# Kernel optimization log

Measured on AMD Instinct MI355X. Metric: run time of the kernel, lower is better.

Reference implementation:

```python
import jax, jax.numpy as jnp
import numpy as np

B, S, D, H = 2, 2048, 1024, 16
DK = D // H


def setup_inputs() -> dict:
    key = jax.random.key(0)
    ks = jax.random.split(key, 12)
    scale = 1.0 / np.sqrt(D)
    inp = {
        "Q": jax.random.normal(ks[0], (B, S, D), jnp.float32),
        "K": jax.random.normal(ks[1], (B, S, D), jnp.float32),
        "V": jax.random.normal(ks[2], (B, S, D), jnp.float32),
        "mask": jnp.tril(jnp.ones((S, S), jnp.int32))[None, None],  # [1,1,S,S] causal
        "Wq": jax.random.normal(ks[3], (D, D), jnp.float32) * scale,
        "bq": jnp.zeros((D,), jnp.float32),
        "Wk": jax.random.normal(ks[4], (D, D), jnp.float32) * scale,
        "bk": jnp.zeros((D,), jnp.float32),
        "Wv": jax.random.normal(ks[5], (D, D), jnp.float32) * scale,
        "bv": jnp.zeros((D,), jnp.float32),
        "Wo": jax.random.normal(ks[6], (D, D), jnp.float32) * scale,
        "bo": jnp.zeros((D,), jnp.float32),
    }
    return inp


def _split_heads(x):
    # [B,S,D] -> [B,H,S,DK]
    b, s, _ = x.shape
    return x.reshape(b, s, H, DK).transpose(0, 2, 1, 3)


def reference(Q, K, V, mask, Wq, bq, Wk, bk, Wv, bv, Wo, bo):
    # Linear projections (torch Linear: x @ W.T + b)
    q = _split_heads(Q @ Wq.T + bq)
    k = _split_heads(K @ Wk.T + bk)
    v = _split_heads(V @ Wv.T + bv)
    scores = jnp.einsum("bhqd,bhkd->bhqk", q, k) / np.sqrt(DK).astype(np.float32)
    scores = jnp.where(mask == 0, jnp.float32(-1e9), scores)
    attn = jax.nn.softmax(scores, axis=-1)
    out = jnp.einsum("bhqk,bhkd->bhqd", attn, v)
    out = out.transpose(0, 2, 1, 3).reshape(Q.shape[0], Q.shape[1], D)  # combine heads
    out = out @ Wo.T + bo
    return out, attn
```

## Files before the change

kernel.cpp:

```cpp
#include <hip/hip_runtime.h>
#include <hip/hip_bf16.h>
#include <math.h>

#define B_ 2
#define S_ 2048
#define D_ 1024
#define H_ 16
#define DK_ 64

typedef __bf16 bf16_t;
typedef __bf16 bf16x8 __attribute__((ext_vector_type(8)));
typedef __bf16 bf16x4 __attribute__((ext_vector_type(4)));
typedef float f32x4 __attribute__((ext_vector_type(4)));

__device__ __forceinline__ void gload_lds16(const void* g, void* l) {
    __builtin_amdgcn_global_load_lds(
        (const __attribute__((address_space(1))) unsigned int*)g,
        (__attribute__((address_space(3))) unsigned int*)l, 16, 0, 0);
}

__global__ __launch_bounds__(256) void cvt_kernel(
    const float* __restrict__ Q, const float* __restrict__ K, const float* __restrict__ V,
    const float* __restrict__ Wq, const float* __restrict__ Wk,
    const float* __restrict__ Wv, const float* __restrict__ Wo,
    bf16_t* __restrict__ dst)
{
    int gid = blockIdx.x * 256 + threadIdx.x;
    for (int i = gid; i < 2097152; i += 2048 * 256) {
        const float* src;
        size_t soff;
        if (i < 1572864) {
            int s = i >> 19;
            src = (s == 0) ? Q : (s == 1) ? K : V;
            soff = (size_t)(i - (s << 19)) * 8;
        } else {
            int j = i - 1572864;
            int s = j >> 17;
            src = (s == 0) ? Wq : (s == 1) ? Wk : (s == 2) ? Wv : Wo;
            soff = (size_t)(j & 131071) * 8;
        }
        float4 a = *(const float4*)(src + soff);
        float4 b = *(const float4*)(src + soff + 4);
        bf16x8 o;
        o[0] = (bf16_t)a.x; o[1] = (bf16_t)a.y; o[2] = (bf16_t)a.z; o[3] = (bf16_t)a.w;
        o[4] = (bf16_t)b.x; o[5] = (bf16_t)b.y; o[6] = (bf16_t)b.z; o[7] = (bf16_t)b.w;
        *(bf16x8*)(dst + (size_t)i * 8) = o;
    }
}

__global__ __launch_bounds__(256) void qkv_gemm_kernel(
    const bf16_t* __restrict__ xq, const bf16_t* __restrict__ xk, const bf16_t* __restrict__ xv,
    const bf16_t* __restrict__ wqb, const bf16_t* __restrict__ wkb, const bf16_t* __restrict__ wvb,
    const float* __restrict__ bq, const float* __restrict__ bk, const float* __restrict__ bv,
    bf16_t* __restrict__ qws, bf16_t* __restrict__ kws, bf16_t* __restrict__ vws)
{
    __shared__ __align__(16) bf16_t As[2][128 * 32];
    __shared__ __align__(16) bf16_t Bs[2][128 * 32];

    const int z = blockIdx.z;
    const bf16_t* A  = (z == 0) ? xq : (z == 1) ? xk : xv;
    const bf16_t* Wb = (z == 0) ? wqb : (z == 1) ? wkb : wvb;
    const float* bias = (z == 0) ? bq : (z == 1) ? bk : bv;
    bf16_t* out       = (z == 0) ? qws : (z == 1) ? kws : vws;

    const int tid = threadIdx.x;
    const int lane = tid & 63, w = tid >> 6;
    const int lr = lane & 15, lg = lane >> 4;
    const int wr = w >> 1, wc = w & 1;
    const int m0 = blockIdx.y * 128, n0 = blockIdx.x * 128;
    const int sr = lane >> 2;
    const int sc = (lane & 3) * 8;

    f32x4 acc[4][4] = {};

    auto stage = [&](int p, int kt) {
        #pragma unroll
        for (int i = 0; i < 2; ++i) {
            int row = w * 32 + i * 16;
            gload_lds16(&A[(size_t)(m0 + row + sr) * 1024 + kt + sc], &As[p][row * 32]);
            gload_lds16(&Wb[(size_t)(n0 + row + sr) * 1024 + kt + sc], &Bs[p][row * 32]);
        }
    };

    stage(0, 0);
    __syncthreads();
    int p = 0;
    for (int kt = 0; kt < 1024; kt += 32) {
        if (kt + 32 < 1024) stage(p ^ 1, kt + 32);
        bf16x8 af[4], bfr[4];
        #pragma unroll
        for (int mi = 0; mi < 4; ++mi)
            af[mi] = *(const bf16x8*)&As[p][(wr * 64 + mi * 16 + lr) * 32 + lg * 8];
        #pragma unroll
        for (int ni = 0; ni < 4; ++ni)
            bfr[ni] = *(const bf16x8*)&Bs[p][(wc * 64 + ni * 16 + lr) * 32 + lg * 8];
        #pragma unroll
        for (int mi = 0; mi < 4; ++mi)
            #pragma unroll
            for (int ni = 0; ni < 4; ++ni)
                acc[mi][ni] = __builtin_amdgcn_mfma_f32_16x16x32_bf16(af[mi], bfr[ni], acc[mi][ni], 0, 0, 0);
        __syncthreads();
        p ^= 1;
    }

    #pragma unroll
    for (int mi = 0; mi < 4; ++mi) {
        int mrow = m0 + wr * 64 + mi * 16 + lg * 4;
        #pragma unroll
        for (int ni = 0; ni < 4; ++ni) {
            int n = n0 + wc * 64 + ni * 16 + lr;
            float bvl = bias[n];
            int h = n >> 6, dk = n & 63;
            #pragma unroll
            for (int r = 0; r < 4; ++r) {
                int m = mrow + r;
                int b = m >> 11, s = m & 2047;
                float val = acc[mi][ni][r] + bvl;
                if (z < 2) {
                    out[(((size_t)(b * H_ + h)) * S_ + s) * DK_ + dk] = (bf16_t)val;
                } else {
                    out[(((size_t)(b * H_ + h)) * DK_ + dk) * S_ + s] = (bf16_t)val;
                }
            }
        }
    }
}

__global__ __launch_bounds__(256, 2) void attn_kernel(
    const bf16_t* __restrict__ qws, const bf16_t* __restrict__ kws, const bf16_t* __restrict__ vws,
    float* __restrict__ attn_out, bf16_t* __restrict__ ctx)
{
    __shared__ __align__(16) bf16_t Ks[2][64][72];
    __shared__ __align__(16) bf16_t Vs[2][64][72];
    __shared__ __align__(16) bf16_t Ps[4][16][72];
    __shared__ __align__(16) float  Ps32[4][16][68];

    const int tid = threadIdx.x;
    const int lane = tid & 63, w = tid >> 6;
    const int lr = lane & 15, lg = lane >> 4;

    const int fid = blockIdx.x;
    const int xcd = fid & 7;
    const int slot = fid >> 3;
    const int bh = xcd * 4 + (slot >> 4);
    const int pr = slot & 15;
    const int b = bh >> 4, h = bh & 15;

    const bf16_t* qh = qws + (size_t)bh * S_ * DK_;
    const bf16_t* kh = kws + (size_t)bh * S_ * DK_;
    const bf16_t* vh = vws + (size_t)bh * DK_ * S_;
    float* ab = attn_out + (size_t)bh * S_ * S_;

    const float SCALE2 = 0.18033688011112042f;

    const int srow = tid >> 3;
    const int scol = (tid & 7) * 8;

    const int prow = lane >> 4;
    const int pcol = (lane & 15) * 4;

    #pragma unroll
    for (int half = 0; half < 2; ++half) {
        const int qt = half ? pr : 31 - pr;
        const int q0 = qt * 64;
        const int nt = qt + 1;
        const int qrow = q0 + w * 16 + lr;

        bf16x8 qf0 = *(const bf16x8*)&qh[(size_t)qrow * DK_ + lg * 8];
        bf16x8 qf1 = *(const bf16x8*)&qh[(size_t)qrow * DK_ + 32 + lg * 8];

        {
            uint4 c0 = *(const uint4*)&kh[(size_t)srow * DK_ + scol];
            uint4 c1 = *(const uint4*)&kh[(size_t)(srow + 32) * DK_ + scol];
            *(uint4*)&Ks[0][srow][scol] = c0;
            *(uint4*)&Ks[0][srow + 32][scol] = c1;
        }
        __syncthreads();
        int p = 0;
        float l = 0.0f;
        for (int t = 0; t < nt; ++t) {
            const bool pre = (t + 1 < nt);
            uint4 k0n, k1n;
            if (pre) {
                k0n = *(const uint4*)&kh[(size_t)((t + 1) * 64 + srow) * DK_ + scol];
                k1n = *(const uint4*)&kh[(size_t)((t + 1) * 64 + srow + 32) * DK_ + scol];
            }
            f32x4 sf[4] = {};
            #pragma unroll
            for (int fj = 0; fj < 4; ++fj) {
                bf16x8 a0 = *(const bf16x8*)&Ks[p][fj * 16 + lr][lg * 8];
                bf16x8 a1 = *(const bf16x8*)&Ks[p][fj * 16 + lr][32 + lg * 8];
                sf[fj] = __builtin_amdgcn_mfma_f32_16x16x32_bf16(a0, qf0, sf[fj], 0, 0, 0);
                sf[fj] = __builtin_amdgcn_mfma_f32_16x16x32_bf16(a1, qf1, sf[fj], 0, 0, 0);
            }
            if (t == qt) {
                #pragma unroll
                for (int fj = 0; fj < 4; ++fj)
                    #pragma unroll
                    for (int r = 0; r < 4; ++r) {
                        float s2 = sf[fj][r] * SCALE2;
                        if (t * 64 + fj * 16 + lg * 4 + r > qrow) s2 = -1e30f;
                        l += exp2f(s2);
                    }
            } else {
                #pragma unroll
                for (int fj = 0; fj < 4; ++fj)
                    #pragma unroll
                    for (int r = 0; r < 4; ++r)
                        l += exp2f(sf[fj][r] * SCALE2);
            }
            if (pre) {
                *(uint4*)&Ks[p ^ 1][srow][scol] = k0n;
                *(uint4*)&Ks[p ^ 1][srow + 32][scol] = k1n;
            }
            __syncthreads();
            p ^= 1;
        }
        l += __shfl_xor(l, 16, 64);
        l += __shfl_xor(l, 32, 64);
        const float csub = log2f(l);

        {
            uint4 c0 = *(const uint4*)&kh[(size_t)srow * DK_ + scol];
            uint4 c1 = *(const uint4*)&kh[(size_t)(srow + 32) * DK_ + scol];
            uint4 d0 = *(const uint4*)&vh[(size_t)srow * S_ + scol];
            uint4 d1 = *(const uint4*)&vh[(size_t)(srow + 32) * S_ + scol];
            *(uint4*)&Ks[0][srow][scol] = c0;
            *(uint4*)&Ks[0][srow + 32][scol] = c1;
            *(uint4*)&Vs[0][srow][scol] = d0;
            *(uint4*)&Vs[0][srow + 32][scol] = d1;
        }
        __syncthreads();
        p = 0;
        f32x4 oacc[4] = {};
        for (int t = 0; t < nt; ++t) {
            const bool pre = (t + 1 < nt);
            uint4 k0n, k1n, v0n, v1n;
            if (pre) {
                k0n = *(const uint4*)&kh[(size_t)((t + 1) * 64 + srow) * DK_ + scol];
                k1n = *(const uint4*)&kh[(size_t)((t + 1) * 64 + srow + 32) * DK_ + scol];
                v0n = *(const uint4*)&vh[(size_t)srow * S_ + (t + 1) * 64 + scol];
                v1n = *(const uint4*)&vh[(size_t)(srow + 32) * S_ + (t + 1) * 64 + scol];
            }
            f32x4 sf[4] = {};
            #pragma unroll
            for (int fj = 0; fj < 4; ++fj) {
                bf16x8 a0 = *(const bf16x8*)&Ks[p][fj * 16 + lr][lg * 8];
                bf16x8 a1 = *(const bf16x8*)&Ks[p][fj * 16 + lr][32 + lg * 8];
                sf[fj] = __builtin_amdgcn_mfma_f32_16x16x32_bf16(a0, qf0, sf[fj], 0, 0, 0);
                sf[fj] = __builtin_amdgcn_mfma_f32_16x16x32_bf16(a1, qf1, sf[fj], 0, 0, 0);
            }
            const bool diag = (t == qt);
            #pragma unroll
            for (int fj = 0; fj < 4; ++fj) {
                f32x4 pv;
                #pragma unroll
                for (int r = 0; r < 4; ++r) {
                    float s2 = sf[fj][r] * SCALE2;
                    if (diag && (t * 64 + fj * 16 + lg * 4 + r > qrow)) s2 = -1e30f;
                    pv[r] = exp2f(s2 - csub);
                }
                *(f32x4*)&Ps32[w][lr][fj * 16 + lg * 4] = pv;
                bf16x4 pb;
                #pragma unroll
                for (int r = 0; r < 4; ++r) pb[r] = (bf16_t)pv[r];
                *(bf16x4*)&Ps[w][lr][fj * 16 + lg * 4] = pb;
            }
            #pragma unroll
            for (int i = 0; i < 4; ++i) {
                int row = prow + i * 4;
                f32x4 pvt = *(const f32x4*)&Ps32[w][row][pcol];
                __builtin_nontemporal_store(pvt,
                    (f32x4*)&ab[(size_t)(q0 + w * 16 + row) * S_ + t * 64 + pcol]);
            }
            #pragma unroll
            for (int ks = 0; ks < 2; ++ks) {
                bf16x8 ap = *(const bf16x8*)&Ps[w][lr][ks * 32 + lg * 8];
                #pragma unroll
                for (int fd = 0; fd < 4; ++fd) {
                    bf16x8 bv = *(const bf16x8*)&Vs[p][fd * 16 + lr][ks * 32 + lg * 8];
                    oacc[fd] = __builtin_amdgcn_mfma_f32_16x16x32_bf16(ap, bv, oacc[fd], 0, 0, 0);
                }
            }
            if (pre) {
                *(uint4*)&Ks[p ^ 1][srow][scol] = k0n;
                *(uint4*)&Ks[p ^ 1][srow + 32][scol] = k1n;
                *(uint4*)&Vs[p ^ 1][srow][scol] = v0n;
                *(uint4*)&Vs[p ^ 1][srow + 32][scol] = v1n;
            }
            __syncthreads();
            p ^= 1;
        }

        {
            int zc4 = (S_ - nt * 64) >> 2;
            if (zc4 > 0) {
                f32x4 z4 = {};
                for (int i = tid; i < 64 * zc4; i += 256) {
                    int row = i / zc4, c = i % zc4;
                    __builtin_nontemporal_store(z4, (f32x4*)&ab[(size_t)(q0 + row) * S_ + nt * 64 + c * 4]);
                }
            }
        }

        const int qrow2 = q0 + w * 16 + lg * 4;
        #pragma unroll
        for (int fd = 0; fd < 4; ++fd) {
            #pragma unroll
            for (int r = 0; r < 4; ++r) {
                int s = qrow2 + r;
                int d = h * 64 + fd * 16 + lr;
                ctx[((size_t)(b * S_ + s)) * D_ + d] = (bf16_t)oacc[fd][r];
            }
        }
        __syncthreads();
    }
}

__global__ __launch_bounds__(256) void out_gemm_kernel(
    const bf16_t* __restrict__ A, const bf16_t* __restrict__ Wb,
    const float* __restrict__ bias, float* __restrict__ out)
{
    __shared__ __align__(16) bf16_t As[2][128 * 32];
    __shared__ __align__(16) bf16_t Bs[2][64 * 32];

    const int tid = threadIdx.x;
    const int lane = tid & 63, w = tid >> 6;
    const int lr = lane & 15, lg = lane >> 4;
    const int wr = w >> 1, wc = w & 1;
    const int m0 = blockIdx.y * 128, n0 = blockIdx.x * 64;
    const int sr = lane >> 2;
    const int sc = (lane & 3) * 8;

    f32x4 acc[4][2] = {};

    auto stage = [&](int p, int kt) {
        #pragma unroll
        for (int i = 0; i < 2; ++i) {
            int row = w * 32 + i * 16;
            gload_lds16(&A[(size_t)(m0 + row + sr) * 1024 + kt + sc], &As[p][row * 32]);
        }
        int brow = w * 16;
        gload_lds16(&Wb[(size_t)(n0 + brow + sr) * 1024 + kt + sc], &Bs[p][brow * 32]);
    };

    stage(0, 0);
    __syncthreads();
    int p = 0;
    for (int kt = 0; kt < 1024; kt += 32) {
        if (kt + 32 < 1024) stage(p ^ 1, kt + 32);
        bf16x8 af[4], bfr[2];
        #pragma unroll
        for (int mi = 0; mi < 4; ++mi)
            af[mi] = *(const bf16x8*)&As[p][(wr * 64 + mi * 16 + lr) * 32 + lg * 8];
        #pragma unroll
        for (int ni = 0; ni < 2; ++ni)
            bfr[ni] = *(const bf16x8*)&Bs[p][(wc * 32 + ni * 16 + lr) * 32 + lg * 8];
        #pragma unroll
        for (int mi = 0; mi < 4; ++mi)
            #pragma unroll
            for (int ni = 0; ni < 2; ++ni)
                acc[mi][ni] = __builtin_amdgcn_mfma_f32_16x16x32_bf16(af[mi], bfr[ni], acc[mi][ni], 0, 0, 0);
        __syncthreads();
        p ^= 1;
    }

    #pragma unroll
    for (int mi = 0; mi < 4; ++mi) {
        int mrow = m0 + wr * 64 + mi * 16 + lg * 4;
        #pragma unroll
        for (int ni = 0; ni < 2; ++ni) {
            int n = n0 + wc * 32 + ni * 16 + lr;
            float bvl = bias[n];
            #pragma unroll
            for (int r = 0; r < 4; ++r) {
                int m = mrow + r;
                out[(size_t)m * D_ + n] = acc[mi][ni][r] + bvl;
            }
        }
    }
}

extern "C" void kernel_launch(void* const* d_in, const int* in_sizes, int n_in,
                              void* d_out, int out_size, void* d_ws, size_t ws_size,
                              hipStream_t stream) {
    const float* Q   = (const float*)d_in[0];
    const float* Kin = (const float*)d_in[1];
    const float* V   = (const float*)d_in[2];
    const float* Wq = (const float*)d_in[4];
    const float* bq = (const float*)d_in[5];
    const float* Wk = (const float*)d_in[6];
    const float* bk = (const float*)d_in[7];
    const float* Wv = (const float*)d_in[8];
    const float* bv = (const float*)d_in[9];
    const float* Wo = (const float*)d_in[10];
    const float* bo = (const float*)d_in[11];

    float* out_ptr  = (float*)d_out;
    float* attn_ptr = out_ptr + (size_t)B_ * S_ * D_;

    const size_t E4M = 4194304;
    bf16_t* base = (bf16_t*)d_ws;
    bf16_t* qws = base;
    bf16_t* kws = base + E4M;
    bf16_t* vws = base + 2 * E4M;
    bf16_t* ctx = base + 3 * E4M;
    bf16_t* cvt = base + 4 * E4M;
    bf16_t* xq  = cvt;
    bf16_t* xk  = cvt + E4M;
    bf16_t* xv  = cvt + 2 * E4M;
    bf16_t* wqb = cvt + 3 * E4M;
    bf16_t* wkb = wqb + 1048576;
    bf16_t* wvb = wkb + 1048576;
    bf16_t* wob = wvb + 1048576;

    dim3 blk(256);
    cvt_kernel<<<dim3(2048), blk, 0, stream>>>(Q, Kin, V, Wq, Wk, Wv, Wo, cvt);
    qkv_gemm_kernel<<<dim3(8, 32, 3), blk, 0, stream>>>(
        xq, xk, xv, wqb, wkb, wvb, bq, bk, bv, qws, kws, vws);
    attn_kernel<<<dim3(512), blk, 0, stream>>>(qws, kws, vws, attn_ptr, ctx);
    out_gemm_kernel<<<dim3(16, 32), blk, 0, stream>>>(ctx, wob, bo, out_ptr);
}
```

Before: 225.7 us.

## Split attention into separate row-sum and output passes via global buffer

```diff
diff --git a/kernel.cpp b/kernel.cpp
--- a/kernel.cpp
+++ b/kernel.cpp
@@ -126,14 +126,11 @@
     }
 }
 
-__global__ __launch_bounds__(256, 2) void attn_kernel(
-    const bf16_t* __restrict__ qws, const bf16_t* __restrict__ kws, const bf16_t* __restrict__ vws,
-    float* __restrict__ attn_out, bf16_t* __restrict__ ctx)
+__global__ __launch_bounds__(256, 2) void attn_pass1_kernel(
+    const bf16_t* __restrict__ qws, const bf16_t* __restrict__ kws,
+    float* __restrict__ lbuf)
 {
     __shared__ __align__(16) bf16_t Ks[2][64][72];
-    __shared__ __align__(16) bf16_t Vs[2][64][72];
-    __shared__ __align__(16) bf16_t Ps[4][16][72];
-    __shared__ __align__(16) float  Ps32[4][16][68];
 
     const int tid = threadIdx.x;
     const int lane = tid & 63, w = tid >> 6;
@@ -144,20 +141,14 @@
     const int slot = fid >> 3;
     const int bh = xcd * 4 + (slot >> 4);
     const int pr = slot & 15;
-    const int b = bh >> 4, h = bh & 15;
 
     const bf16_t* qh = qws + (size_t)bh * S_ * DK_;
     const bf16_t* kh = kws + (size_t)bh * S_ * DK_;
-    const bf16_t* vh = vws + (size_t)bh * DK_ * S_;
-    float* ab = attn_out + (size_t)bh * S_ * S_;
 
     const float SCALE2 = 0.18033688011112042f;
 
     const int srow = tid >> 3;
     const int scol = (tid & 7) * 8;
-
-    const int prow = lane >> 4;
-    const int pcol = (lane & 15) * 4;
 
     #pragma unroll
     for (int half = 0; half < 2; ++half) {
@@ -218,7 +209,53 @@
         }
         l += __shfl_xor(l, 16, 64);
         l += __shfl_xor(l, 32, 64);
-        const float csub = log2f(l);
+        if (lg == 0) lbuf[(size_t)bh * S_ + qrow] = log2f(l);
+        __syncthreads();
+    }
+}
+
+__global__ __launch_bounds__(256, 2) void attn_pass2_kernel(
+    const bf16_t* __restrict__ qws, const bf16_t* __restrict__ kws, const bf16_t* __restrict__ vws,
+    const float* __restrict__ lbuf, float* __restrict__ attn_out, bf16_t* __restrict__ ctx)
+{
+    __shared__ __align__(16) bf16_t Ks[2][64][72];
+    __shared__ __align__(16) bf16_t Vs[2][64][72];
+    __shared__ __align__(16) bf16_t Ps[4][16][72];
+    __shared__ __align__(16) float  Ps32[4][16][68];
+
+    const int tid = threadIdx.x;
+    const int lane = tid & 63, w = tid >> 6;
+    const int lr = lane & 15, lg = lane >> 4;
+
+    const int fid = blockIdx.x;
+    const int xcd = fid & 7;
+    const int slot = fid >> 3;
+    const int bh = xcd * 4 + (slot >> 4);
+    const int pr = slot & 15;
+    const int b = bh >> 4, h = bh & 15;
+
+    const bf16_t* qh = qws + (size_t)bh * S_ * DK_;
+    const bf16_t* kh = kws + (size_t)bh * S_ * DK_;
+    const bf16_t* vh = vws + (size_t)bh * DK_ * S_;
+    float* ab = attn_out + (size_t)bh * S_ * S_;
+
+    const float SCALE2 = 0.18033688011112042f;
+
+    const int srow = tid >> 3;
+    const int scol = (tid & 7) * 8;
+    const int prow = lane >> 4;
+    const int pcol = (lane & 15) * 4;
+
+    #pragma unroll
+    for (int half = 0; half < 2; ++half) {
+        const int qt = half ? pr : 31 - pr;
+        const int q0 = qt * 64;
+        const int nt = qt + 1;
+        const int qrow = q0 + w * 16 + lr;
+
+        bf16x8 qf0 = *(const bf16x8*)&qh[(size_t)qrow * DK_ + lg * 8];
+        bf16x8 qf1 = *(const bf16x8*)&qh[(size_t)qrow * DK_ + 32 + lg * 8];
+        const float csub = lbuf[(size_t)bh * S_ + qrow];
 
         {
             uint4 c0 = *(const uint4*)&kh[(size_t)srow * DK_ + scol];
@@ -231,7 +268,7 @@
             *(uint4*)&Vs[0][srow + 32][scol] = d1;
         }
         __syncthreads();
-        p = 0;
+        int p = 0;
         f32x4 oacc[4] = {};
         for (int t = 0; t < nt; ++t) {
             const bool pre = (t + 1 < nt);
@@ -413,11 +450,13 @@
     bf16_t* wkb = wqb + 1048576;
     bf16_t* wvb = wkb + 1048576;
     bf16_t* wob = wvb + 1048576;
+    float*  lbuf = (float*)(wob + 1048576);
 
     dim3 blk(256);
     cvt_kernel<<<dim3(2048), blk, 0, stream>>>(Q, Kin, V, Wq, Wk, Wv, Wo, cvt);
     qkv_gemm_kernel<<<dim3(8, 32, 3), blk, 0, stream>>>(
         xq, xk, xv, wqb, wkb, wvb, bq, bk, bv, qws, kws, vws);
-    attn_kernel<<<dim3(512), blk, 0, stream>>>(qws, kws, vws, attn_ptr, ctx);
+    attn_pass1_kernel<<<dim3(512), blk, 0, stream>>>(qws, kws, lbuf);
+    attn_pass2_kernel<<<dim3(512), blk, 0, stream>>>(qws, kws, vws, lbuf, attn_ptr, ctx);
     out_gemm_kernel<<<dim3(16, 32), blk, 0, stream>>>(ctx, wob, bo, out_ptr);
 }
```

After: 258.3 us. 1.14x slower.
